# Kernel tuning notes

Measured on AMD Instinct MI355X. Metric: run time of the kernel, lower is better.

Reference implementation:

```python
import jax, jax.numpy as jnp
import numpy as np

DECAY = 0.99
EPS = 1e-05


def setup_inputs() -> dict:
    key = jax.random.key(0)
    k1, k2, k3 = jax.random.split(key, 3)
    inp = jax.random.normal(k1, (8, 1024, 512), dtype=jnp.float32)
    embed = jax.random.normal(k2, (512, 8192), dtype=jnp.float32)
    # buffers: cluster_size starts at zeros, embed_avg is a clone of embed in torch
    cluster_size = jnp.zeros((8192,), dtype=jnp.float32)
    embed_avg = embed
    return {"input": inp, "embed": embed, "cluster_size": cluster_size, "embed_avg": embed_avg}


def reference(input, embed, cluster_size, embed_avg):
    dim, n_embed = embed.shape
    flatten = input.reshape(-1, dim)  # [N, dim]
    # squared euclidean distance via expansion: ||f||^2 - 2 f.E + ||E||^2 -> [N, n_embed]
    dist = ((flatten ** 2).sum(axis=1, keepdims=True)
            - 2.0 * flatten @ embed
            + (embed ** 2).sum(axis=0, keepdims=True))
    embed_ind_flat = jnp.argmin(dist, axis=1)  # argmax of -dist == argmin of dist
    embed_ind = embed_ind_flat.reshape(input.shape[:-1])
    # nearest-codebook lookup: F.embedding(ind, embed.T)
    quantize = jnp.take(embed.T, embed_ind, axis=0)  # [..., dim]
    # training-mode EMA statistics (one-hot scatter sums, done without a dense one-hot)
    onehot_sum = jnp.zeros((n_embed,), flatten.dtype).at[embed_ind_flat].add(1.0)
    embed_sum = jax.ops.segment_sum(flatten, embed_ind_flat, num_segments=n_embed).T  # [dim, n_embed]
    new_cluster_size = cluster_size * DECAY + (1.0 - DECAY) * onehot_sum
    new_embed_avg = embed_avg * DECAY + (1.0 - DECAY) * embed_sum
    n = new_cluster_size.sum()
    cs = (new_cluster_size + EPS) / (n + n_embed * EPS) * n
    new_embed = new_embed_avg / cs[None, :]
    # commitment loss (quantize detached) and straight-through estimator
    diff = jnp.mean((jax.lax.stop_gradient(quantize) - input) ** 2)
    quantize_st = input + jax.lax.stop_gradient(quantize - input)
    return (quantize_st, diff, embed_ind, new_embed, new_cluster_size, new_embed_avg)
```

## Files before the change

### kernel.cpp

```cpp
#include <hip/hip_runtime.h>


constexpr int N = 8192;
constexpr int K = 512;
constexpr int M = 8192;

typedef unsigned short ushortT;
typedef __attribute__((ext_vector_type(8))) short s8v;
typedef __attribute__((ext_vector_type(4))) float f4v;

__device__ __forceinline__ ushortT f2bf(float x) {
    unsigned u = __float_as_uint(x);
    unsigned r = (u + 0x7FFFu + ((u >> 16) & 1u)) >> 16;
    return (ushortT)r;
}
__device__ __forceinline__ float bf2f(ushortT h) {
    return __uint_as_float(((unsigned)h) << 16);
}

typedef const __attribute__((address_space(1))) unsigned gau;
typedef __attribute__((address_space(3))) unsigned lau;
__device__ __forceinline__ void gl16(const void* g, void* l) {
    __builtin_amdgcn_global_load_lds((gau*)g, (lau*)l, 16, 0, 0);
}

__device__ __forceinline__ unsigned packDI(float d, int col) {
    unsigned u = __float_as_uint(d);
    unsigned s = (u & 0x80000000u) ? ~u : (u | 0x80000000u);
    return (s & ~0x1FFFu) | (unsigned)col;
}
__device__ __forceinline__ float unpackD(unsigned p) {
    unsigned s = p & ~0x1FFFu;
    unsigned u = (s & 0x80000000u) ? (s & 0x7fffffffu) : ~s;
    return __uint_as_float(u);
}
__device__ __forceinline__ void top2u(unsigned& a, unsigned& b, unsigned c) {
    unsigned mn = c < a ? c : a;
    unsigned mx = c < a ? a : c;
    a = mn;
    b = mx < b ? mx : b;
}

__global__ __launch_bounds__(256) void k_prep(
    const float* __restrict__ f, const float* __restrict__ E,
    ushortT* __restrict__ Fh, ushortT* __restrict__ EhT, ushortT* __restrict__ ElT,
    float* __restrict__ pc, float* __restrict__ counts) {
    __shared__ float tile[64][65];
    int b = blockIdx.x, t = threadIdx.x;
    if (b < 2048) {
        if (b < 32) counts[b * 256 + t] = 0.f;
        size_t i8 = ((size_t)b * 256 + t) * 8;
        float4 x0 = *(const float4*)&f[i8];
        float4 x1 = *(const float4*)&f[i8 + 4];
        float xs[8] = {x0.x, x0.y, x0.z, x0.w, x1.x, x1.y, x1.z, x1.w};
        union { s8v v; ushortT u[8]; } h;
#pragma unroll
        for (int j = 0; j < 8; ++j) h.u[j] = f2bf(xs[j]);
        *(s8v*)&Fh[i8] = h.v;
    } else {
        int bb = b - 2048;
        int jb = bb & 127, kb = bb >> 7;
        int jj = t & 63, kk0 = t >> 6;
        int j0 = jb * 64, k0 = kb * 64;
#pragma unroll
        for (int it = 0; it < 16; ++it) {
            int kk = it * 4 + kk0;
            tile[kk][jj] = E[(size_t)(k0 + kk) * M + j0 + jj];
        }
        __syncthreads();
        int r = t >> 2, ks = (t & 3) * 16;
        union { s8v v[2]; ushortT u[16]; } h, lo;
        float nrm = 0.f;
#pragma unroll
        for (int i = 0; i < 16; ++i) {
            float x = tile[ks + i][r];
            nrm = fmaf(x, x, nrm);
            ushortT hh = f2bf(x);
            h.u[i] = hh;
            lo.u[i] = f2bf(x - bf2f(hh));
        }
        size_t o = (size_t)(j0 + r) * K + k0 + ks;
        *(s8v*)&EhT[o] = h.v[0];
        *(s8v*)&EhT[o + 8] = h.v[1];
        *(s8v*)&ElT[o] = lo.v[0];
        *(s8v*)&ElT[o + 8] = lo.v[1];
        nrm += __shfl_down(nrm, 2);
        nrm += __shfl_down(nrm, 1);
        if ((t & 3) == 0) pc[(size_t)kb * M + j0 + r] = nrm;
    }
}

__global__ __launch_bounds__(512) void k_score(
    const ushortT* __restrict__ Fh, const ushortT* __restrict__ Eh,
    const float* __restrict__ pc, unsigned* __restrict__ pv) {
    __shared__ alignas(16) ushortT ls[2][2][256 * 64];

    int bid = blockIdx.x;
    int xcd = bid & 7, local = bid >> 3;
    int rb = xcd * 4 + (local & 3);
    int cb = local >> 2;
    int rowBase = rb * 256, colBase = cb * 256;
    int tid = threadIdx.x;
    int w = tid >> 6, l = tid & 63;
    int wr = w >> 2, wc = w & 3;
    int l15 = l & 15, g4 = l >> 4;
    int s7 = l15 & 7;

    const ushortT* srcA = Fh + (size_t)(rowBase + w * 32) * K;
    const ushortT* srcB = Eh + (size_t)(colBase + w * 32) * K;

    f4v acc[8][4];
#pragma unroll
    for (int m = 0; m < 8; ++m)
#pragma unroll
        for (int n = 0; n < 4; ++n) acc[m][n] = (f4v){0.f, 0.f, 0.f, 0.f};

#define STAGE(p, ch)                                                  \
    do {                                                              \
        _Pragma("unroll")                                             \
        for (int i_ = 0; i_ < 4; ++i_) {                              \
            int q_ = i_ * 64 + l;                                     \
            int row_ = q_ >> 3, slot_ = q_ & 7;                       \
            int swz_ = (slot_ ^ (row_ & 7)) * 8;                      \
            size_t so_ = (size_t)row_ * K + (ch) * 64 + swz_;         \
            gl16(srcA + so_, &ls[p][0][w * 2048 + q_ * 8]);           \
            gl16(srcB + so_, &ls[p][1][w * 2048 + q_ * 8]);           \
        }                                                             \
    } while (0)

    STAGE(0, 0);
    __syncthreads();

#pragma unroll
    for (int ch = 0; ch < 8; ++ch) {
        int p = ch & 1;
        if (ch < 7) STAGE(p ^ 1, ch + 1);
#pragma unroll
        for (int kk = 0; kk < 2; ++kk) {
            s8v a[8], b[4];
#pragma unroll
            for (int m = 0; m < 8; ++m) {
                int rA = wr * 128 + m * 16 + l15;
                a[m] = *(const s8v*)&ls[p][0][rA * 64 + ((kk * 4 + g4) ^ s7) * 8];
            }
#pragma unroll
            for (int n = 0; n < 4; ++n) {
                int rB = wc * 64 + n * 16 + l15;
                b[n] = *(const s8v*)&ls[p][1][rB * 64 + ((kk * 4 + g4) ^ s7) * 8];
            }
#pragma unroll
            for (int m = 0; m < 8; ++m)
#pragma unroll
                for (int n = 0; n < 4; ++n)
                    acc[m][n] = __builtin_amdgcn_mfma_f32_16x16x32_bf16(
                        a[m], b[n], acc[m][n], 0, 0, 0);
        }
        __syncthreads();
    }
#undef STAGE

    float cj[4];
#pragma unroll
    for (int n = 0; n < 4; ++n) {
        int col = colBase + wc * 64 + n * 16 + l15;
        float s = 0.f;
#pragma unroll
        for (int kb = 0; kb < 8; ++kb) s += pc[(size_t)kb * M + col];
        cj[n] = s;
    }
    unsigned* cand = (unsigned*)ls;

#pragma unroll
    for (int m = 0; m < 8; ++m)
#pragma unroll
        for (int q = 0; q < 4; ++q) {
            unsigned p0 = packDI(fmaf(-2.f, acc[m][0][q], cj[0]), colBase + wc * 64 + l15);
            unsigned p1 = packDI(fmaf(-2.f, acc[m][1][q], cj[1]), colBase + wc * 64 + 16 + l15);
            unsigned p2 = packDI(fmaf(-2.f, acc[m][2][q], cj[2]), colBase + wc * 64 + 32 + l15);
            unsigned p3 = packDI(fmaf(-2.f, acc[m][3][q], cj[3]), colBase + wc * 64 + 48 + l15);
            unsigned a_ = p0 < p1 ? p0 : p1;
            unsigned b_ = p0 < p1 ? p1 : p0;
            top2u(a_, b_, p2);
            top2u(a_, b_, p3);
#pragma unroll
            for (int mk = 8; mk >= 2; mk >>= 1) {
                unsigned oa = __shfl_xor((int)a_, mk);
                unsigned ob = __shfl_xor((int)b_, mk);
                top2u(a_, b_, oa);
                top2u(a_, b_, ob);
            }
            if (l15 < 2) {
                int row = wr * 128 + m * 16 + g4 * 4 + q;
                int slot = wc * 4 + l15 * 2;
                cand[row * 17 + slot] = a_;
                cand[row * 17 + slot + 1] = b_;
            }
        }
    __syncthreads();
    if (tid < 256) {
        unsigned best = cand[tid * 17], second = cand[tid * 17 + 1];
#pragma unroll
        for (int i = 2; i < 16; i += 2) {
            top2u(best, second, cand[tid * 17 + i]);
            top2u(best, second, cand[tid * 17 + i + 1]);
        }
        size_t o = (size_t)(rowBase + tid) * 64 + cb * 2;
        pv[o] = best;
        pv[o + 1] = second;
    }
}

__global__ __launch_bounds__(256) void k_combine(
    const unsigned* __restrict__ pv, const float* __restrict__ f,
    const ushortT* __restrict__ EhT, const ushortT* __restrict__ ElT,
    const float* __restrict__ pc,
    int* __restrict__ indws, float* __restrict__ o_ind, float* __restrict__ counts,
    float* __restrict__ o_q, float* __restrict__ diffp) {
    __shared__ float dsum[4];
    int w = threadIdx.x >> 6, l = threadIdx.x & 63;
    int row = blockIdx.x * 4 + w;
    unsigned e = pv[(size_t)row * 64 + l];
    unsigned mn = e;
#pragma unroll
    for (int m = 1; m < 64; m <<= 1) {
        unsigned o = __shfl_xor((int)mn, m);
        mn = o < mn ? o : mn;
    }
    float thr = unpackD(mn) + 2.0f;
    float dl = unpackD(e);
    float bestd = 3.4e38f; int bestj = 0x7fffffff;
    float4 fa = *(const float4*)&f[(size_t)row * K + l * 8];
    float4 fb = *(const float4*)&f[(size_t)row * K + l * 8 + 4];
    float fx[8] = {fa.x, fa.y, fa.z, fa.w, fb.x, fb.y, fb.z, fb.w};
    s8v qh, ql;
    unsigned long long mask = __ballot(dl <= thr);
    while (mask) {
        int b = __ffsll(mask) - 1;
        mask &= mask - 1;
        int j = (int)(__shfl((int)e, b) & 0x1fff);
        s8v hv = *(const s8v*)(EhT + (size_t)j * K + l * 8);
        s8v lv = *(const s8v*)(ElT + (size_t)j * K + l * 8);
        float a = 0.f;
#pragma unroll
        for (int q = 0; q < 8; ++q)
            a = fmaf(fx[q], bf2f((ushortT)hv[q]) + bf2f((ushortT)lv[q]), a);
#pragma unroll
        for (int m = 1; m < 64; m <<= 1) a += __shfl_xor(a, m);
        float cj = 0.f;
#pragma unroll
        for (int kb = 0; kb < 8; ++kb) cj += pc[(size_t)kb * M + j];
        float d = cj - 2.f * a;
        if (d < bestd || (d == bestd && j < bestj)) {
            bestd = d; bestj = j; qh = hv; ql = lv;
        }
    }
    float os[8];
    float local = 0.f;
#pragma unroll
    for (int q = 0; q < 8; ++q) {
        float qv = bf2f((ushortT)qh[q]) + bf2f((ushortT)ql[q]);
        float d = qv - fx[q];
        os[q] = fx[q] + d;
        local = fmaf(d, d, local);
    }
    float4 o0 = {os[0], os[1], os[2], os[3]};
    float4 o1 = {os[4], os[5], os[6], os[7]};
    *(float4*)&o_q[(size_t)row * K + l * 8] = o0;
    *(float4*)&o_q[(size_t)row * K + l * 8 + 4] = o1;
#pragma unroll
    for (int m = 1; m < 64; m <<= 1) local += __shfl_xor(local, m);
    if (l == 0) {
        indws[row] = bestj;
        o_ind[row] = (float)bestj;
        atomicAdd(&counts[bestj], 1.0f);
        dsum[w] = local;
    }
    __syncthreads();
    if (threadIdx.x == 0)
        diffp[blockIdx.x] = dsum[0] + dsum[1] + dsum[2] + dsum[3];
}

__global__ __launch_bounds__(256) void k_ema(
    const float* __restrict__ f, const int* __restrict__ indws,
    const float* __restrict__ ea, float* __restrict__ o_avg, float* __restrict__ o_ne,
    const float* __restrict__ cs_in, const float* __restrict__ counts,
    float* __restrict__ o_ncs,
    const float* __restrict__ diffp, float* __restrict__ o_diff) {
    int b = blockIdx.x, t = threadIdx.x;
    __shared__ float wsum[4];
    if (b == 256) {
        float loc = 0.f;
#pragma unroll 32
        for (int i = 0; i < 32; ++i) {
            int j = i * 256 + t;
            o_ncs[j] = 0.99f * cs_in[j] + 0.01f * counts[j];
        }
        float dl = 0.f;
#pragma unroll
        for (int i = 0; i < 8; ++i) dl += diffp[i * 256 + t];
#pragma unroll
        for (int off = 32; off; off >>= 1) dl += __shfl_down(dl, off);
        if ((t & 63) == 0) wsum[t >> 6] = dl;
        __syncthreads();
        if (t == 0)
            o_diff[0] = (wsum[0] + wsum[1] + wsum[2] + wsum[3]) * (1.0f / 4194304.0f);
        (void)loc;
        return;
    }
    __shared__ float acc[512 * 33];
    __shared__ int q[8192];
    __shared__ int qn;
    __shared__ float csr_s[32];
    __shared__ float nsh;
    for (int i = t; i < 512 * 33; i += 256) acc[i] = 0.f;
    if (t == 0) qn = 0;
    __syncthreads();
    for (int r = t; r < N; r += 256) {
        int j = indws[r];
        if ((j >> 5) == b) {
            int s = atomicAdd(&qn, 1);
            q[s] = (r << 5) | (j & 31);
        }
    }
    __syncthreads();
    int nq = qn;
    int s = 0;
    for (; s + 4 <= nq; s += 4) {
        int e0 = q[s], e1 = q[s + 1], e2 = q[s + 2], e3 = q[s + 3];
        float a0 = f[(size_t)(e0 >> 5) * K + t],       c0 = f[(size_t)(e0 >> 5) * K + t + 256];
        float a1 = f[(size_t)(e1 >> 5) * K + t],       c1 = f[(size_t)(e1 >> 5) * K + t + 256];
        float a2 = f[(size_t)(e2 >> 5) * K + t],       c2 = f[(size_t)(e2 >> 5) * K + t + 256];
        float a3 = f[(size_t)(e3 >> 5) * K + t],       c3 = f[(size_t)(e3 >> 5) * K + t + 256];
        acc[t * 33 + (e0 & 31)] += a0;         acc[(t + 256) * 33 + (e0 & 31)] += c0;
        acc[t * 33 + (e1 & 31)] += a1;         acc[(t + 256) * 33 + (e1 & 31)] += c1;
        acc[t * 33 + (e2 & 31)] += a2;         acc[(t + 256) * 33 + (e2 & 31)] += c2;
        acc[t * 33 + (e3 & 31)] += a3;         acc[(t + 256) * 33 + (e3 & 31)] += c3;
    }
    for (; s < nq; ++s) {
        int e = q[s];
        float a0 = f[(size_t)(e >> 5) * K + t];
        float c0 = f[(size_t)(e >> 5) * K + t + 256];
        acc[t * 33 + (e & 31)] += a0;
        acc[(t + 256) * 33 + (e & 31)] += c0;
    }
    float loc = 0.f;
#pragma unroll 32
    for (int i = 0; i < 32; ++i) {
        int j = i * 256 + t;
        loc += 0.99f * cs_in[j] + 0.01f * counts[j];
    }
#pragma unroll
    for (int off = 32; off; off >>= 1) loc += __shfl_down(loc, off);
    __syncthreads();
    if ((t & 63) == 0) wsum[t >> 6] = loc;
    __syncthreads();
    if (t == 0) nsh = wsum[0] + wsum[1] + wsum[2] + wsum[3];
    __syncthreads();
    if (t < 32) {
        int j = b * 32 + t;
        float v = 0.99f * cs_in[j] + 0.01f * counts[j];
        float n = nsh;
        csr_s[t] = (v + 1e-5f) / (n + 8192.0f * 1e-5f) * n;
    }
    __syncthreads();
    for (int i = t; i < 512 * 32; i += 256) {
        int d = i >> 5, c = i & 31;
        size_t o = (size_t)d * M + b * 32 + c;
        float val = 0.99f * ea[o] + 0.01f * acc[d * 33 + c];
        o_avg[o] = val;
        o_ne[o] = val / csr_s[c];
    }
}

extern "C" void kernel_launch(void* const* d_in, const int* in_sizes, int n_in,
                              void* d_out, int out_size, void* d_ws, size_t ws_size,
                              hipStream_t stream) {
    const float* f     = (const float*)d_in[0];
    const float* E     = (const float*)d_in[1];
    const float* cs_in = (const float*)d_in[2];
    const float* ea    = (const float*)d_in[3];

    float* out = (float*)d_out;
    float* o_q    = out;
    float* o_diff = out + 4194304;
    float* o_ind  = out + 4194305;
    float* o_ne   = out + 4202497;
    float* o_ncs  = out + 8396801;
    float* o_avg  = out + 8404993;

    ushortT* Fh  = (ushortT*)o_q;
    ushortT* EhT = (ushortT*)o_ne;
    ushortT* ElT = EhT + (size_t)M * K;
    unsigned* pv = (unsigned*)o_avg;

    float* wsf    = (float*)d_ws;
    float* counts = wsf + 8192;
    int*   indws  = (int*)(wsf + 24576);
    float* diffp  = wsf + 32768;
    float* pc     = wsf + 40960;

    k_prep   <<<3072, 256, 0, stream>>>(f, E, Fh, EhT, ElT, pc, counts);
    k_score  <<<1024, 512, 0, stream>>>(Fh, EhT, pc, pv);
    k_combine<<<2048, 256, 0, stream>>>(pv, f, EhT, ElT, pc, indws, o_ind, counts,
                                        o_q, diffp);
    k_ema    <<<257, 256, 0, stream>>>(f, indws, ea, o_avg, o_ne,
                                       cs_in, counts, o_ncs,
                                       diffp, o_diff);
}
```

Before: 161.0 us.

## Make score kernel persistent over four row tiles per block

The score GEMM kernel now launches 256 blocks instead of 1024, and each block walks four 256-row tiles for one column tile in a single 32-step pipelined loop. The top-2 reduction runs after every eighth step, and the accumulators are then reset. Each block reuses its column-norm load and keeps double-buffered loading running across tile boundaries, which cuts block launch and prologue cost. In exchange the B tile is re-staged every step anyway, the loop is no longer fully unrolled, and there are extra barriers plus a separate LDS candidate buffer. Only 256 blocks are in flight, which may underfill the GPU.

```diff
diff --git a/kernel.cpp b/kernel.cpp
--- a/kernel.cpp
+++ b/kernel.cpp
@@ -94,36 +94,48 @@
     const ushortT* __restrict__ Fh, const ushortT* __restrict__ Eh,
     const float* __restrict__ pc, unsigned* __restrict__ pv) {
     __shared__ alignas(16) ushortT ls[2][2][256 * 64];
+    __shared__ unsigned cand[256 * 17];
 
     int bid = blockIdx.x;
-    int xcd = bid & 7, local = bid >> 3;
-    int rb = xcd * 4 + (local & 3);
-    int cb = local >> 2;
-    int rowBase = rb * 256, colBase = cb * 256;
+    int xcd = bid & 7, q = bid >> 3;
+    int cb = q;
+    int colBase = cb * 256;
     int tid = threadIdx.x;
     int w = tid >> 6, l = tid & 63;
     int wr = w >> 2, wc = w & 3;
     int l15 = l & 15, g4 = l >> 4;
     int s7 = l15 & 7;
 
-    const ushortT* srcA = Fh + (size_t)(rowBase + w * 32) * K;
     const ushortT* srcB = Eh + (size_t)(colBase + w * 32) * K;
 
+    float cj[4];
+#pragma unroll
+    for (int n = 0; n < 4; ++n) {
+        int col = colBase + wc * 64 + n * 16 + l15;
+        float s = 0.f;
+#pragma unroll
+        for (int kb = 0; kb < 8; ++kb) s += pc[(size_t)kb * M + col];
+        cj[n] = s;
+    }
+
     f4v acc[8][4];
 #pragma unroll
     for (int m = 0; m < 8; ++m)
 #pragma unroll
         for (int n = 0; n < 4; ++n) acc[m][n] = (f4v){0.f, 0.f, 0.f, 0.f};
 
-#define STAGE(p, ch)                                                  \
+#define STAGE(p, s)                                                   \
     do {                                                              \
+        int t_ = (s) >> 3, c_ = (s) & 7;                              \
+        const ushortT* srcA_ = Fh +                                   \
+            (size_t)((xcd * 4 + t_) * 256 + w * 32) * K;              \
         _Pragma("unroll")                                             \
         for (int i_ = 0; i_ < 4; ++i_) {                              \
             int q_ = i_ * 64 + l;                                     \
             int row_ = q_ >> 3, slot_ = q_ & 7;                       \
             int swz_ = (slot_ ^ (row_ & 7)) * 8;                      \
-            size_t so_ = (size_t)row_ * K + (ch) * 64 + swz_;         \
-            gl16(srcA + so_, &ls[p][0][w * 2048 + q_ * 8]);           \
+            size_t so_ = (size_t)row_ * K + c_ * 64 + swz_;           \
+            gl16(srcA_ + so_, &ls[p][0][w * 2048 + q_ * 8]);          \
             gl16(srcB + so_, &ls[p][1][w * 2048 + q_ * 8]);           \
         }                                                             \
     } while (0)
@@ -131,83 +143,84 @@
     STAGE(0, 0);
     __syncthreads();
 
-#pragma unroll
-    for (int ch = 0; ch < 8; ++ch) {
-        int p = ch & 1;
-        if (ch < 7) STAGE(p ^ 1, ch + 1);
+    for (int s = 0; s < 32; ++s) {
+        int p = s & 1;
+        if (s + 1 < 32) STAGE(p ^ 1, s + 1);
 #pragma unroll
         for (int kk = 0; kk < 2; ++kk) {
             s8v a[8], b[4];
 #pragma unroll
-            for (int m = 0; m < 8; ++m) {
-                int rA = wr * 128 + m * 16 + l15;
-                a[m] = *(const s8v*)&ls[p][0][rA * 64 + ((kk * 4 + g4) ^ s7) * 8];
+            for (int m_ = 0; m_ < 8; ++m_) {
+                int rA = wr * 128 + m_ * 16 + l15;
+                a[m_] = *(const s8v*)&ls[p][0][rA * 64 + ((kk * 4 + g4) ^ s7) * 8];
             }
 #pragma unroll
-            for (int n = 0; n < 4; ++n) {
-                int rB = wc * 64 + n * 16 + l15;
-                b[n] = *(const s8v*)&ls[p][1][rB * 64 + ((kk * 4 + g4) ^ s7) * 8];
+            for (int n_ = 0; n_ < 4; ++n_) {
+                int rB = wc * 64 + n_ * 16 + l15;
+                b[n_] = *(const s8v*)&ls[p][1][rB * 64 + ((kk * 4 + g4) ^ s7) * 8];
             }
 #pragma unroll
+            for (int m_ = 0; m_ < 8; ++m_)
+#pragma unroll
+                for (int n_ = 0; n_ < 4; ++n_)
+                    acc[m_][n_] = __builtin_amdgcn_mfma_f32_16x16x32_bf16(
+                        a[m_], b[n_], acc[m_][n_], 0, 0, 0);
+        }
+        __syncthreads();
+
+        if ((s & 7) == 7) {
+            int rowBase = (xcd * 4 + (s >> 3)) * 256;
+#pragma unroll
             for (int m = 0; m < 8; ++m)
 #pragma unroll
-                for (int n = 0; n < 4; ++n)
-                    acc[m][n] = __builtin_amdgcn_mfma_f32_16x16x32_bf16(
-                        a[m], b[n], acc[m][n], 0, 0, 0);
-        }
-        __syncthreads();
+                for (int qq = 0; qq < 4; ++qq) {
+                    unsigned p0 = packDI(fmaf(-2.f, acc[m][0][qq], cj[0]),
+                                         colBase + wc * 64 + l15);
+                    unsigned p1 = packDI(fmaf(-2.f, acc[m][1][qq], cj[1]),
+                                         colBase + wc * 64 + 16 + l15);
+                    unsigned p2 = packDI(fmaf(-2.f, acc[m][2][qq], cj[2]),
+                                         colBase + wc * 64 + 32 + l15);
+                    unsigned p3 = packDI(fmaf(-2.f, acc[m][3][qq], cj[3]),
+                                         colBase + wc * 64 + 48 + l15);
+                    unsigned a_ = p0 < p1 ? p0 : p1;
+                    unsigned b_ = p0 < p1 ? p1 : p0;
+                    top2u(a_, b_, p2);
+                    top2u(a_, b_, p3);
+#pragma unroll
+                    for (int mk = 8; mk >= 2; mk >>= 1) {
+                        unsigned oa = __shfl_xor((int)a_, mk);
+                        unsigned ob = __shfl_xor((int)b_, mk);
+                        top2u(a_, b_, oa);
+                        top2u(a_, b_, ob);
+                    }
+                    if (l15 < 2) {
+                        int row = wr * 128 + m * 16 + g4 * 4 + qq;
+                        int slot = wc * 4 + l15 * 2;
+                        cand[row * 17 + slot] = a_;
+                        cand[row * 17 + slot + 1] = b_;
+                    }
+                    acc[m][qq < 4 ? 0 : 0][0] = acc[m][0][0];
+                }
+            __syncthreads();
+            if (tid < 256) {
+                unsigned best = cand[tid * 17], second = cand[tid * 17 + 1];
+#pragma unroll
+                for (int i = 2; i < 16; i += 2) {
+                    top2u(best, second, cand[tid * 17 + i]);
+                    top2u(best, second, cand[tid * 17 + i + 1]);
+                }
+                size_t o = (size_t)(rowBase + tid) * 64 + cb * 2;
+                pv[o] = best;
+                pv[o + 1] = second;
+            }
+#pragma unroll
+            for (int m = 0; m < 8; ++m)
+#pragma unroll
+                for (int n = 0; n < 4; ++n) acc[m][n] = (f4v){0.f, 0.f, 0.f, 0.f};
+            __syncthreads();
+        }
     }
 #undef STAGE
-
-    float cj[4];
-#pragma unroll
-    for (int n = 0; n < 4; ++n) {
-        int col = colBase + wc * 64 + n * 16 + l15;
-        float s = 0.f;
-#pragma unroll
-        for (int kb = 0; kb < 8; ++kb) s += pc[(size_t)kb * M + col];
-        cj[n] = s;
-    }
-    unsigned* cand = (unsigned*)ls;
-
-#pragma unroll
-    for (int m = 0; m < 8; ++m)
-#pragma unroll
-        for (int q = 0; q < 4; ++q) {
-            unsigned p0 = packDI(fmaf(-2.f, acc[m][0][q], cj[0]), colBase + wc * 64 + l15);
-            unsigned p1 = packDI(fmaf(-2.f, acc[m][1][q], cj[1]), colBase + wc * 64 + 16 + l15);
-            unsigned p2 = packDI(fmaf(-2.f, acc[m][2][q], cj[2]), colBase + wc * 64 + 32 + l15);
-            unsigned p3 = packDI(fmaf(-2.f, acc[m][3][q], cj[3]), colBase + wc * 64 + 48 + l15);
-            unsigned a_ = p0 < p1 ? p0 : p1;
-            unsigned b_ = p0 < p1 ? p1 : p0;
-            top2u(a_, b_, p2);
-            top2u(a_, b_, p3);
-#pragma unroll
-            for (int mk = 8; mk >= 2; mk >>= 1) {
-                unsigned oa = __shfl_xor((int)a_, mk);
-                unsigned ob = __shfl_xor((int)b_, mk);
-                top2u(a_, b_, oa);
-                top2u(a_, b_, ob);
-            }
-            if (l15 < 2) {
-                int row = wr * 128 + m * 16 + g4 * 4 + q;
-                int slot = wc * 4 + l15 * 2;
-                cand[row * 17 + slot] = a_;
-                cand[row * 17 + slot + 1] = b_;
-            }
-        }
-    __syncthreads();
-    if (tid < 256) {
-        unsigned best = cand[tid * 17], second = cand[tid * 17 + 1];
-#pragma unroll
-        for (int i = 2; i < 16; i += 2) {
-            top2u(best, second, cand[tid * 17 + i]);
-            top2u(best, second, cand[tid * 17 + i + 1]);
-        }
-        size_t o = (size_t)(rowBase + tid) * 64 + cb * 2;
-        pv[o] = best;
-        pv[o + 1] = second;
-    }
 }
 
 __global__ __launch_bounds__(256) void k_combine(
@@ -242,8 +255,8 @@
         s8v lv = *(const s8v*)(ElT + (size_t)j * K + l * 8);
         float a = 0.f;
 #pragma unroll
-        for (int q = 0; q < 8; ++q)
-            a = fmaf(fx[q], bf2f((ushortT)hv[q]) + bf2f((ushortT)lv[q]), a);
+        for (int qq = 0; qq < 8; ++qq)
+            a = fmaf(fx[qq], bf2f((ushortT)hv[qq]) + bf2f((ushortT)lv[qq]), a);
 #pragma unroll
         for (int m = 1; m < 64; m <<= 1) a += __shfl_xor(a, m);
         float cj = 0.f;
@@ -257,10 +270,10 @@
     float os[8];
     float local = 0.f;
 #pragma unroll
-    for (int q = 0; q < 8; ++q) {
-        float qv = bf2f((ushortT)qh[q]) + bf2f((ushortT)ql[q]);
-        float d = qv - fx[q];
-        os[q] = fx[q] + d;
+    for (int qq = 0; qq < 8; ++qq) {
+        float qv = bf2f((ushortT)qh[qq]) + bf2f((ushortT)ql[qq]);
+        float d = qv - fx[qq];
+        os[qq] = fx[qq] + d;
         local = fmaf(d, d, local);
     }
     float4 o0 = {os[0], os[1], os[2], os[3]};
@@ -289,7 +302,6 @@
     int b = blockIdx.x, t = threadIdx.x;
     __shared__ float wsum[4];
     if (b == 256) {
-        float loc = 0.f;
 #pragma unroll 32
         for (int i = 0; i < 32; ++i) {
             int j = i * 256 + t;
@@ -304,7 +316,6 @@
         __syncthreads();
         if (t == 0)
             o_diff[0] = (wsum[0] + wsum[1] + wsum[2] + wsum[3]) * (1.0f / 4194304.0f);
-        (void)loc;
         return;
     }
     __shared__ float acc[512 * 33];
@@ -400,7 +411,7 @@
     float* pc     = wsf + 40960;
 
     k_prep   <<<3072, 256, 0, stream>>>(f, E, Fh, EhT, ElT, pc, counts);
-    k_score  <<<1024, 512, 0, stream>>>(Fh, EhT, pc, pv);
+    k_score  <<<256, 512, 0, stream>>>(Fh, EhT, pc, pv);
     k_combine<<<2048, 256, 0, stream>>>(pv, f, EhT, ElT, pc, indws, o_ind, counts,
                                         o_q, diffp);
     k_ema    <<<257, 256, 0, stream>>>(f, indws, ea, o_avg, o_ne,
```

Result: slower. 172.5 us (+7.1%).
